# Kernel tuning notes

Hardware: AMD Instinct MI355X
Metric: run time of the kernel (lower is better)

Reference implementation:

```python
import jax, jax.numpy as jnp
import numpy as np

B, C, H, W = 2, 64, 256, 256
P = 3          # n_pyramids
NO = 16        # per-pyramid output channels
FEX = P * NO   # 48
N = 32768      # |yi| = mask.sum()


def _conv(x, w):
    return jax.lax.conv_general_dilated(
        x, w, window_strides=(1, 1), padding='SAME',
        dimension_numbers=('NCHW', 'OIHW', 'NCHW'))


def _mask_weight(mask):
    # MaskedConv: w = mask / clamp(avg3x3(mask), 1e-8)  (computed under no_grad)
    avg = jnp.ones((1, 1, 3, 3), mask.dtype) / 9.0
    wm = _conv(mask, avg)
    return jax.lax.stop_gradient(mask / jnp.clip(wm, 1e-8))


def _mconv(x, w, wm):
    return _conv(x, w) * wm


def _resblock(x, w1, w2, mask, wm):
    x = mask * x
    r = jax.nn.relu(_mconv(x, w1, wm))
    r = _mconv(r, w2, wm)
    return x + r


def setup_inputs() -> dict:
    key = jax.random.key(0)
    ks = jax.random.split(key, 12)
    rng = np.random.default_rng(0)
    yi_np = np.sort(rng.choice(H * W, size=N, replace=False)).astype(np.int32)
    mask_flat = np.zeros(H * W, np.float32)
    mask_flat[yi_np] = 1.0
    mask = jnp.asarray(mask_flat).reshape(1, 1, H, W)
    # near-identity homography (3x3)
    m = jnp.asarray(np.array([[0.9, 0.05, 2.0],
                              [-0.03, 1.1, -1.0],
                              [1e-4, -2e-4, 1.0]], np.float32))
    s = 0.05
    return {
        'xs': jax.random.normal(ks[0], (P, B, C, H, W), jnp.float32),
        'mask': mask,
        'yi': jnp.asarray(yi_np),
        'm': m,
        'ss_res_w': s * jax.random.normal(ks[1], (P, 2, 2, C, C, 3, 3), jnp.float32),
        'ss_out_w': s * jax.random.normal(ks[2], (P, NO, C, 3, 3), jnp.float32),
        'feat_res_w': s * jax.random.normal(ks[3], (2, 2, FEX, FEX, 3, 3), jnp.float32),
        'samp_w1': s * jax.random.normal(ks[4], (FEX, FEX + 1), jnp.float32),
        'samp_b1': s * jax.random.normal(ks[5], (FEX,), jnp.float32),
        'samp_w2': s * jax.random.normal(ks[6], (FEX, FEX), jnp.float32),
        'samp_b2': s * jax.random.normal(ks[7], (FEX,), jnp.float32),
        'samp_w3': s * jax.random.normal(ks[8], (P, FEX), jnp.float32),
        'samp_b3': s * jax.random.normal(ks[9], (P,), jnp.float32),
    }


def reference(xs, mask, yi, m, ss_res_w, ss_out_w, feat_res_w,
              samp_w1, samp_b1, samp_w2, samp_b2, samp_w3, samp_b3):
    wm = _mask_weight(mask)
    # ---- MSResFeature: per-pyramid MaskedResSeq(64->64->16, depth=3) ----
    feats = []
    for i in range(P):  # small fixed loop over pyramids
        x = mask * xs[i]
        x = _resblock(x, ss_res_w[i, 0, 0], ss_res_w[i, 0, 1], mask, wm)
        x = _resblock(x, ss_res_w[i, 1, 0], ss_res_w[i, 1, 1], mask, wm)
        x = _mconv(x, ss_out_w[i], wm)
        feats.append(x)
    f = jnp.concatenate(feats, axis=1)  # (B, 48, H, W)
    # shared trunk: MaskedResSeq(48->48->48, depth=3), residual
    g = mask * f
    g = _resblock(g, feat_res_w[0, 0], feat_res_w[0, 1], mask, wm)
    g = _resblock(g, feat_res_w[1, 0], feat_res_w[1, 1], mask, wm)
    f = f + g
    b = f.shape[0]
    # ---- gather at sparse indices yi ----
    ff = f.reshape(b, FEX, -1)[:, :, yi]  # (B, 48, N)
    # ---- dsda: |Jacobian det| of projective warp, log-scaled (no_grad) ----
    ygrid, xgrid = jnp.meshgrid(jnp.arange(H, dtype=f.dtype),
                                jnp.arange(W, dtype=f.dtype), indexing='ij')
    wcoord = m[2, 0] * xgrid + m[2, 1] * ygrid + m[2, 2]
    dsda = jnp.abs(jnp.linalg.det(m)) / jnp.clip(jnp.abs(wcoord), 1e-8) ** 3
    dsda = jnp.log(dsda.reshape(-1)[yi] + 1e-8)
    dsda = jax.lax.stop_gradient(jnp.broadcast_to(dsda[None, None, :], (b, 1, N)))
    h = jnp.concatenate((ff, dsda), axis=1)  # (B, 49, N)
    # ---- 1x1 Conv1d sampler MLP ----
    h = jax.nn.relu(jnp.einsum('oc,bcn->bon', samp_w1, h) + samp_b1[None, :, None])
    h = jax.nn.relu(jnp.einsum('oc,bcn->bon', samp_w2, h) + samp_b2[None, :, None])
    p = jnp.einsum('oc,bcn->bon', samp_w3, h) + samp_b3[None, :, None]  # (B, 3, N)
    # ---- scatter back to dense grid and blend pyramids ----
    ws = jnp.zeros((b, P, H * W), f.dtype).at[:, :, yi].set(p)
    ws = ws.reshape(b, P, H, W)
    out = jnp.sum(ws.transpose(1, 0, 2, 3)[:, :, None] * xs, axis=0)  # (B, C, H, W)
    return out
```

## Files before the change

kernel.cpp:

```cpp
#include <hip/hip_runtime.h>
#include <hip/hip_bf16.h>

typedef unsigned short ushort_t;
typedef __attribute__((ext_vector_type(8))) short short8;
typedef __attribute__((ext_vector_type(4))) short short4v;
typedef __attribute__((ext_vector_type(4))) float f32x4;

constexpr int Hh = 256, Ww = 256, HW = Hh * Ww;
constexpr int Bb = 2, Cc = 64, Pp = 3, NOo = 16, FEXc = 48, Nn = 32768;
constexpr int TW = 32, TH = 4;
constexpr int HALOP4 = 6 * 34;
constexpr int ASLOT = 26;
constexpr int PADH = 72;

__device__ inline ushort_t f2bf(float v) {
    __hip_bfloat16 h = __float2bfloat16(v);
    return *(ushort_t*)&h;
}
__device__ inline float bf2f(ushort_t u) {
    __hip_bfloat16 h = *(__hip_bfloat16*)&u;
    return __bfloat162float(h);
}
__device__ inline void gload_lds16(const ushort_t* g, ushort_t* l) {
    __builtin_amdgcn_global_load_lds(
        (const __attribute__((address_space(1))) unsigned int*)g,
        (__attribute__((address_space(3))) unsigned int*)l, 16, 0, 0);
}
template <int N>
__device__ __forceinline__ void wait_vm() {
    if constexpr (N == 0) asm volatile("s_waitcnt vmcnt(0)" ::: "memory");
    else if constexpr (N == 3) asm volatile("s_waitcnt vmcnt(3)" ::: "memory");
    else if constexpr (N == 5) asm volatile("s_waitcnt vmcnt(5)" ::: "memory");
}

__global__ __launch_bounds__(256) void k_wm(const float* __restrict__ mask,
                                            float* __restrict__ wm,
                                            float* __restrict__ zpage) {
    int pos = blockIdx.x * 256 + threadIdx.x;
    if (blockIdx.x == 0 && threadIdx.x < 64) zpage[threadIdx.x] = 0.f;
    int h = pos >> 8, w = pos & 255;
    float s = 0.f;
    #pragma unroll
    for (int dy = -1; dy <= 1; ++dy)
        #pragma unroll
        for (int dx = -1; dx <= 1; ++dx) {
            int hh = h + dy, ww = w + dx;
            if (hh >= 0 && hh < Hh && ww >= 0 && ww < Ww) s += mask[hh * Ww + ww];
        }
    float avg = s * (1.f / 9.f);
    wm[pos] = mask[pos] / fmaxf(avg, 1e-8f);
}

__global__ __launch_bounds__(256) void k_zero(float4* __restrict__ p) {
    p[blockIdx.x * 256 + threadIdx.x] = make_float4(0.f, 0.f, 0.f, 0.f);
}

__global__ __launch_bounds__(256) void k_wx_res(const float* __restrict__ src,
                                                ushort_t* __restrict__ dst) {
    int idx = blockIdx.x * 256 + threadIdx.x;
    int j = idx / 36864; int rem = idx - j * 36864;
    int t = rem >> 12; int o = (rem >> 6) & 63; int c = rem & 63;
    dst[idx] = f2bf(src[j * 36864 + o * 576 + c * 9 + t]);
}
__global__ __launch_bounds__(256) void k_wx_out(const float* __restrict__ src,
                                                ushort_t* __restrict__ dst) {
    int idx = blockIdx.x * 256 + threadIdx.x;
    int i = idx / 9216; int rem = idx - i * 9216;
    int t = rem >> 10; int o = (rem >> 6) & 15; int c = rem & 63;
    dst[idx] = f2bf(src[i * 9216 + o * 576 + c * 9 + t]);
}
__global__ __launch_bounds__(256) void k_wx_trunk(const float* __restrict__ src,
                                                  ushort_t* __restrict__ dst) {
    int idx = blockIdx.x * 256 + threadIdx.x;
    int j = idx / 27648; int rem = idx - j * 27648;
    int t = rem / 3072; int rem2 = rem - t * 3072;
    int o = rem2 >> 6; int c = rem2 & 63;
    float v = (c < 48) ? src[j * (48 * 48 * 9) + o * 432 + c * 9 + t] : 0.f;
    dst[idx] = f2bf(v);
}
__global__ __launch_bounds__(256) void k_wx_mlp(
    const float* __restrict__ w1, const float* __restrict__ b1,
    const float* __restrict__ w2, const float* __restrict__ b2,
    const float* __restrict__ w3, const float* __restrict__ b3,
    ushort_t* __restrict__ dst) {
    int idx = blockIdx.x * 256 + threadIdx.x;
    float v = 0.f;
    if (idx < 3072) {
        int o = idx >> 6, c = idx & 63;
        v = (c < 49) ? w1[o * 49 + c] : (c == 49 ? b1[o] : 0.f);
    } else if (idx < 6144) {
        int o = (idx - 3072) >> 6, c = idx & 63;
        v = (c < 48) ? w2[o * 48 + c] : (c == 48 ? b2[o] : 0.f);
    } else {
        int o = (idx - 6144) >> 6, c = idx & 63;
        if (o < 3) v = (c < 48) ? w3[o * 48 + c] : (c == 49 ? b3[o] : 0.f);
    }
    dst[idx] = f2bf(v);
}

__global__ __launch_bounds__(256) void k_xm(const float* __restrict__ xs,
                                            const float* __restrict__ mask,
                                            ushort_t* __restrict__ X) {
    __shared__ float l[64 * 65];
    const int p0 = blockIdx.x * 64;
    const size_t zoff = (size_t)blockIdx.y * 64 * HW;
    const int tid = threadIdx.x;
    const int px = tid & 63;
    const float mv = mask[p0 + px];
    #pragma unroll
    for (int k = 0; k < 16; ++k) {
        int c = (tid >> 6) + 4 * k;
        l[c * 65 + px] = xs[zoff + (size_t)c * HW + p0 + px] * mv;
    }
    __syncthreads();
    #pragma unroll
    for (int k = 0; k < 2; ++k) {
        int idx = tid + k * 256;
        int p = idx >> 3, c8 = idx & 7;
        short8 v;
        #pragma unroll
        for (int i = 0; i < 8; ++i) v[i] = (short)f2bf(l[(c8 * 8 + i) * 65 + p]);
        *(short8*)&X[zoff + (size_t)(p0 + p) * 64 + c8 * 8] = v;
    }
}

template <int OC, int MODE, bool TOF>
__global__ __launch_bounds__(256) void k_mconv(
    const ushort_t* __restrict__ in,
    const ushort_t* __restrict__ wgt, int wstride,
    const float* __restrict__ wm,
    const ushort_t* __restrict__ zp,
    const ushort_t* __restrict__ base,
    ushort_t* __restrict__ out) {
    constexpr int NG = (OC + 31) / 32;
    constexpr int NPH = 2 * NG;
    constexpr int WSLOT = (OC >= 48) ? 20 : 12;
    constexpr int WV = WSLOT / 4;
    extern __shared__ __align__(1024) ushort_t smem[];
    ushort_t* alds  = smem;
    ushort_t* wlds0 = smem + 208 * 64;
    ushort_t* wlds1 = wlds0 + WSLOT * 512;
    const int tid = threadIdx.x;
    const int wv = tid >> 6;
    const int ln = tid & 63;
    const int w0 = blockIdx.x * TW, h0 = blockIdx.y * TH;
    const int zz = blockIdx.z;
    const ushort_t* inb = in + (size_t)zz * HW * 64;
    const ushort_t* wB = wgt + (size_t)(zz >> 1) * wstride;
    const ushort_t* baseb = base ? base + (size_t)zz * HW * 64 : nullptr;
    ushort_t* outb = TOF ? out + (size_t)(zz & 1) * HW * 64 : out + (size_t)zz * HW * 64;
    const int ocb = TOF ? (zz >> 1) * 16 : 0;
    const int lo = ln & 15, slr = ln >> 4;

    auto wstage = [&](int p, ushort_t* wbuf) {
        const int gi = p >> 1, h = p & 1;
        const int ob = gi * 32;
        const int ocg = (OC - ob >= 32) ? 32 : 16;
        #pragma unroll
        for (int k = 0; k < WV; ++k) {
            int s = wv + 4 * k;
            int rl = s * 16 + (ln >> 2);
            int d = ln & 3;
            int j = d ^ ((rl ^ (rl >> 2)) & 3);
            int t, ol;
            if (ocg == 32) { t = rl >> 5; ol = rl & 31; }
            else           { t = rl >> 4; ol = rl & 15; }
            bool valid = rl < 9 * ocg;
            const ushort_t* src = valid
                ? wB + (size_t)(t * OC + ob + ol) * 64 + h * 32 + j * 8
                : wB + j * 8;
            gload_lds16(src, &wbuf[s * 512]);
        }
    };

    wstage(0, wlds0);
    #pragma unroll
    for (int k = 0; k < 7; ++k) {
        int s = wv + 4 * k;
        if (s < ASLOT) {
            int pp = s * 8 + (ln >> 3);
            int r = (pp * 241) >> 13;
            int col = pp - r * 34;
            int gh = h0 + r - 1, gw = w0 + col - 1;
            bool ok = (pp < HALOP4) & (gh >= 0) & (gh < Hh) & (gw >= 0) & (gw < Ww);
            int che = ((ln & 7) ^ (pp & 7)) << 3;
            const ushort_t* src = ok ? inb + (size_t)(gh * Ww + gw) * 64 + che : zp + che;
            gload_lds16(src, &alds[s * 512]);
        }
    }

    f32x4 acc[2][2];
    #pragma unroll
    for (int p = 0; p < NPH; ++p) {
        const int gi = p >> 1, h = p & 1;
        const int ob = gi * 32;
        const int ocg = (OC - ob >= 32) ? 32 : 16;
        const int nmg = ocg / 16;
        ushort_t* wcur = (p & 1) ? wlds1 : wlds0;
        if (p + 1 < NPH) {
            wstage(p + 1, (p & 1) ? wlds0 : wlds1);
            wait_vm<WV>();
        } else {
            wait_vm<0>();
        }
        __syncthreads();

        if (h == 0) {
            #pragma unroll
            for (int mfl = 0; mfl < 2; ++mfl)
                #pragma unroll
                for (int nf = 0; nf < 2; ++nf) acc[mfl][nf] = (f32x4){0.f, 0.f, 0.f, 0.f};
        }

        #pragma unroll
        for (int dy = 0; dy < 3; ++dy)
            #pragma unroll
            for (int dx = 0; dx < 3; ++dx) {
                const int t = dy * 3 + dx;
                short8 afr[2];
                #pragma unroll
                for (int mfl = 0; mfl < 2; ++mfl) if (mfl < nmg) {
                    int rl = t * ocg + mfl * 16 + lo;
                    afr[mfl] = *(const short8*)
                        &wcur[rl * 32 + ((slr ^ ((rl ^ (rl >> 2)) & 3)) << 3)];
                }
                short8 bfr[2];
                #pragma unroll
                for (int nf = 0; nf < 2; ++nf) {
                    int pp2 = (wv + dy) * 34 + nf * 16 + lo + dx;
                    bfr[nf] = *(const short8*)
                        &alds[pp2 * 64 + (((h * 4 + slr) ^ (pp2 & 7)) << 3)];
                }
                #pragma unroll
                for (int mfl = 0; mfl < 2; ++mfl) if (mfl < nmg)
                    #pragma unroll
                    for (int nf = 0; nf < 2; ++nf)
                        acc[mfl][nf] = __builtin_amdgcn_mfma_f32_16x16x32_bf16(
                            afr[mfl], bfr[nf], acc[mfl][nf], 0, 0, 0);
            }

        if (h == 1) {
            #pragma unroll
            for (int nf = 0; nf < 2; ++nf) {
                int r = h0 + wv;
                int x = w0 + nf * 16 + lo;
                int pos = r * Ww + x;
                float wmv = wm[pos];
                #pragma unroll
                for (int mfl = 0; mfl < 2; ++mfl) if (mfl < nmg) {
                    int o0 = ocb + ob + mfl * 16 + slr * 4;
                    size_t oi = (size_t)pos * 64 + o0;
                    float v[4];
                    #pragma unroll
                    for (int q = 0; q < 4; ++q) v[q] = acc[mfl][nf][q] * wmv;
                    if (MODE == 0) {
                        #pragma unroll
                        for (int q = 0; q < 4; ++q) v[q] = fmaxf(v[q], 0.f);
                    } else if (MODE == 1) {
                        short4v bv = *(const short4v*)&baseb[oi];
                        #pragma unroll
                        for (int q = 0; q < 4; ++q) v[q] += bf2f((ushort_t)bv[q]);
                    }
                    short4v sv;
                    #pragma unroll
                    for (int q = 0; q < 4; ++q) sv[q] = (short)f2bf(v[q]);
                    *(short4v*)&outb[oi] = sv;
                }
            }
        }
        if (p + 1 < NPH) __syncthreads();
    }
}

__global__ __launch_bounds__(256) void k_gather_mlp(
    const ushort_t* __restrict__ F, const ushort_t* __restrict__ G,
    const int* __restrict__ yi, const float* __restrict__ m,
    const ushort_t* __restrict__ wA1, const ushort_t* __restrict__ wA2,
    const ushort_t* __restrict__ wA3, float* __restrict__ pvd) {
    __shared__ __align__(16) ushort_t HA[4 * 16 * PADH];
    __shared__ __align__(16) ushort_t HB[4 * 16 * PADH];
    const int tid = threadIdx.x, wv = tid >> 6, ln = tid & 63;
    ushort_t* ha = HA + wv * 16 * PADH;
    ushort_t* hb = HB + wv * 16 * PADH;
    const int t0 = blockIdx.x * 64 + wv * 16;
    const int b = t0 >> 15;
    const int lo = ln & 15, g8 = (ln >> 4) * 8;

    #pragma unroll
    for (int rnd = 0; rnd < 2; ++rnd) {
        int j = rnd * 64 + ln;
        if (j < 96) {
            int pt = j / 6, sl = j - pt * 6;
            int n = (t0 + pt) & (Nn - 1);
            int pos = yi[n];
            size_t gi = ((size_t)(b * HW) + pos) * 64 + sl * 8;
            short8 fa = *(const short8*)&F[gi];
            short8 ga = *(const short8*)&G[gi];
            short8 sv;
            #pragma unroll
            for (int i = 0; i < 8; ++i)
                sv[i] = (short)f2bf(bf2f((ushort_t)fa[i]) + bf2f((ushort_t)ga[i]));
            *(short8*)&ha[pt * PADH + sl * 8] = sv;
        }
    }
    if (ln < 16) {
        int pt = ln;
        int n = (t0 + pt) & (Nn - 1);
        int pos = yi[n];
        float det = m[0] * (m[4] * m[8] - m[5] * m[7])
                  - m[1] * (m[3] * m[8] - m[5] * m[6])
                  + m[2] * (m[3] * m[7] - m[4] * m[6]);
        int yr = pos >> 8, xc = pos & 255;
        float wc = m[6] * (float)xc + m[7] * (float)yr + m[8];
        float cw = fmaxf(fabsf(wc), 1e-8f);
        float dsda = fabsf(det) / (cw * cw * cw);
        float ld = logf(dsda + 1e-8f);
        const ushort_t one = f2bf(1.0f);
        short8 z = {0, 0, 0, 0, 0, 0, 0, 0};
        short8 sa = z; sa[0] = (short)f2bf(ld); sa[1] = (short)one;
        short8 sb = z; sb[0] = (short)one;
        *(short8*)&ha[pt * PADH + 48] = sa;
        *(short8*)&ha[pt * PADH + 56] = z;
        *(short8*)&hb[pt * PADH + 48] = sb;
        *(short8*)&hb[pt * PADH + 56] = z;
    }
    asm volatile("s_waitcnt lgkmcnt(0)" ::: "memory");

    f32x4 a1[3] = {{0.f,0.f,0.f,0.f},{0.f,0.f,0.f,0.f},{0.f,0.f,0.f,0.f}};
    #pragma unroll
    for (int ks = 0; ks < 2; ++ks) {
        short8 bf = *(const short8*)&ha[lo * PADH + ks * 32 + g8];
        #pragma unroll
        for (int mf = 0; mf < 3; ++mf) {
            short8 af = *(const short8*)&wA1[(mf * 16 + lo) * 64 + ks * 32 + g8];
            a1[mf] = __builtin_amdgcn_mfma_f32_16x16x32_bf16(af, bf, a1[mf], 0, 0, 0);
        }
    }
    #pragma unroll
    for (int mf = 0; mf < 3; ++mf) {
        short4v sv;
        #pragma unroll
        for (int j = 0; j < 4; ++j) sv[j] = (short)f2bf(fmaxf(a1[mf][j], 0.f));
        *(short4v*)&hb[lo * PADH + mf * 16 + (ln >> 4) * 4] = sv;
    }
    asm volatile("s_waitcnt lgkmcnt(0)" ::: "memory");

    f32x4 a2[3] = {{0.f,0.f,0.f,0.f},{0.f,0.f,0.f,0.f},{0.f,0.f,0.f,0.f}};
    #pragma unroll
    for (int ks = 0; ks < 2; ++ks) {
        short8 bf = *(const short8*)&hb[lo * PADH + ks * 32 + g8];
        #pragma unroll
        for (int mf = 0; mf < 3; ++mf) {
            short8 af = *(const short8*)&wA2[(mf * 16 + lo) * 64 + ks * 32 + g8];
            a2[mf] = __builtin_amdgcn_mfma_f32_16x16x32_bf16(af, bf, a2[mf], 0, 0, 0);
        }
    }
    #pragma unroll
    for (int mf = 0; mf < 3; ++mf) {
        short4v sv;
        #pragma unroll
        for (int j = 0; j < 4; ++j) sv[j] = (short)f2bf(fmaxf(a2[mf][j], 0.f));
        *(short4v*)&ha[lo * PADH + mf * 16 + (ln >> 4) * 4] = sv;
    }
    asm volatile("s_waitcnt lgkmcnt(0)" ::: "memory");

    f32x4 a3 = {0.f, 0.f, 0.f, 0.f};
    #pragma unroll
    for (int ks = 0; ks < 2; ++ks) {
        short8 bf = *(const short8*)&ha[lo * PADH + ks * 32 + g8];
        short8 af = *(const short8*)&wA3[lo * 64 + ks * 32 + g8];
        a3 = __builtin_amdgcn_mfma_f32_16x16x32_bf16(af, bf, a3, 0, 0, 0);
    }
    if (ln < 16) {
        int n = (t0 + lo) & (Nn - 1);
        int pos = yi[n];
        #pragma unroll
        for (int j = 0; j < 3; ++j)
            pvd[(size_t)(b * Pp + j) * HW + pos] = a3[j];
    }
}

__global__ __launch_bounds__(256) void k_blend(const float4* __restrict__ xs,
                                               const float4* __restrict__ pvd,
                                               float4* __restrict__ out) {
    int i = blockIdx.x * 256 + threadIdx.x;
    int pos4 = i & (HW / 4 - 1);
    int bc = i >> 14;
    int b = bc >> 6;
    float4 acc = make_float4(0.f, 0.f, 0.f, 0.f);
    #pragma unroll
    for (int p = 0; p < Pp; ++p) {
        float4 pv = pvd[(b * Pp + p) * (HW / 4) + pos4];
        float4 x = xs[p * (Bb * Cc * HW / 4) + i];
        acc.x += pv.x * x.x;
        acc.y += pv.y * x.y;
        acc.z += pv.z * x.z;
        acc.w += pv.w * x.w;
    }
    out[i] = acc;
}

extern "C" void kernel_launch(void* const* d_in, const int* in_sizes, int n_in,
                              void* d_out, int out_size, void* d_ws, size_t ws_size,
                              hipStream_t stream) {
    const float* xs        = (const float*)d_in[0];
    const float* mask      = (const float*)d_in[1];
    const int*   yi        = (const int*)d_in[2];
    const float* m         = (const float*)d_in[3];
    const float* ss_res_w  = (const float*)d_in[4];
    const float* ss_out_w  = (const float*)d_in[5];
    const float* feat_res_w= (const float*)d_in[6];
    const float* w1 = (const float*)d_in[7];
    const float* b1 = (const float*)d_in[8];
    const float* w2 = (const float*)d_in[9];
    const float* b2 = (const float*)d_in[10];
    const float* w3 = (const float*)d_in[11];
    const float* b3 = (const float*)d_in[12];

    float* wm    = (float*)d_ws;
    float* zpage = wm + HW;
    float* pvd   = zpage + 64;
    ushort_t* wB = (ushort_t*)(pvd + (size_t)Bb * Pp * HW);
    constexpr size_t RES_T = 12 * 9 * 64 * 64;
    constexpr size_t OUT_T = 3 * 9 * 16 * 64;
    constexpr size_t TRK_T = 4 * 9 * 48 * 64;
    constexpr size_t MLP_T = 7168;
    constexpr size_t ZT = (size_t)Pp * Bb * HW * 64;
    ushort_t* wA = wB + RES_T + OUT_T + TRK_T;
    ushort_t* X = wA + MLP_T;
    ushort_t* U = X + ZT;
    ushort_t* V = U + ZT;
    ushort_t* F = V + ZT;
    ushort_t* G = F + (size_t)Bb * HW * 64;
    const ushort_t* zp = (const ushort_t*)zpage;

    k_wm<<<HW / 256, 256, 0, stream>>>(mask, wm, zpage);
    k_wx_res  <<<RES_T / 256, 256, 0, stream>>>(ss_res_w, wB);
    k_wx_out  <<<OUT_T / 256, 256, 0, stream>>>(ss_out_w, wB + RES_T);
    k_wx_trunk<<<TRK_T / 256, 256, 0, stream>>>(feat_res_w, wB + RES_T + OUT_T);
    k_wx_mlp  <<<MLP_T / 256, 256, 0, stream>>>(w1, b1, w2, b2, w3, b3, wA);

    const dim3 gridP(Ww / TW, Hh / TH, Pp * Bb);
    const dim3 gridT(Ww / TW, Hh / TH, Bb);
    const int RS = 4 * 9 * 64 * 64;
    const int OS = 9 * 16 * 64;
    constexpr size_t SH64 = 26624 + 2 * 20 * 1024;
    constexpr size_t SH48 = SH64;
    constexpr size_t SH16 = 26624 + 2 * 12 * 1024;

    k_xm<<<dim3(HW / 64, Pp * Bb), 256, 0, stream>>>(xs, mask, X);
    k_mconv<64, 0, false><<<gridP, 256, SH64, stream>>>(X, wB,             RS, wm, zp, nullptr, U);
    k_mconv<64, 1, false><<<gridP, 256, SH64, stream>>>(U, wB + 1 * 36864, RS, wm, zp, X,       V);
    k_mconv<64, 0, false><<<gridP, 256, SH64, stream>>>(V, wB + 2 * 36864, RS, wm, zp, nullptr, U);
    k_mconv<64, 1, false><<<gridP, 256, SH64, stream>>>(U, wB + 3 * 36864, RS, wm, zp, V,       V);
    k_mconv<16, 2, true ><<<gridP, 256, SH16, stream>>>(V, wB + RES_T,     OS, wm, zp, nullptr, F);

    const ushort_t* tw = wB + RES_T + OUT_T;
    k_mconv<48, 0, false><<<gridT, 256, SH48, stream>>>(F, tw,             0, wm, zp, nullptr, U);
    k_mconv<48, 1, false><<<gridT, 256, SH48, stream>>>(U, tw + 1 * 27648, 0, wm, zp, F,       G);
    k_mconv<48, 0, false><<<gridT, 256, SH48, stream>>>(G, tw + 2 * 27648, 0, wm, zp, nullptr, U);
    k_mconv<48, 1, false><<<gridT, 256, SH48, stream>>>(U, tw + 3 * 27648, 0, wm, zp, G,       G);

    k_zero<<<(Bb * Pp * HW / 4) / 256, 256, 0, stream>>>((float4*)pvd);
    k_gather_mlp<<<Bb * Nn / 64, 256, 0, stream>>>(F, G, yi, m,
        wA, wA + 3072, wA + 6144, pvd);
    k_blend<<<(Bb * Cc * HW / 4) / 256, 256, 0, stream>>>((const float4*)xs, (const float4*)pvd,
                                                          (float4*)d_out);
}
```

Measured before the change: 340.1 us.

## Fuse each residual block's two masked convs into one halo-recompute kernel

Adds a k_pair kernel that computes both 3x3 masked convolutions of a residual block in one launch. It loads a 2-pixel halo tile, computes the first conv plus ReLU over the expanded region into LDS, then runs the second conv from LDS and adds the residual read from the staged input. This removes the intermediate global write and read and halves the conv launches. In exchange it recomputes halo work, serializes weight staging (the double-buffered waits become vmcnt(0)), and uses more LDS and accumulator registers per block, which can lower occupancy.

```diff
diff --git a/kernel.cpp b/kernel.cpp
--- a/kernel.cpp
+++ b/kernel.cpp
@@ -11,6 +11,7 @@
 constexpr int TW = 32, TH = 4;
 constexpr int HALOP4 = 6 * 34;
 constexpr int ASLOT = 26;
+constexpr int ITROWS = 288;
 constexpr int PADH = 72;
 
 __device__ inline ushort_t f2bf(float v) {
@@ -26,11 +27,8 @@
         (const __attribute__((address_space(1))) unsigned int*)g,
         (__attribute__((address_space(3))) unsigned int*)l, 16, 0, 0);
 }
-template <int N>
-__device__ __forceinline__ void wait_vm() {
-    if constexpr (N == 0) asm volatile("s_waitcnt vmcnt(0)" ::: "memory");
-    else if constexpr (N == 3) asm volatile("s_waitcnt vmcnt(3)" ::: "memory");
-    else if constexpr (N == 5) asm volatile("s_waitcnt vmcnt(5)" ::: "memory");
+__device__ __forceinline__ void wait_vm0() {
+    asm volatile("s_waitcnt vmcnt(0)" ::: "memory");
 }
 
 __global__ __launch_bounds__(256) void k_wm(const float* __restrict__ mask,
@@ -121,6 +119,198 @@
         #pragma unroll
         for (int i = 0; i < 8; ++i) v[i] = (short)f2bf(l[(c8 * 8 + i) * 65 + p]);
         *(short8*)&X[zoff + (size_t)(p0 + p) * 64 + c8 * 8] = v;
+    }
+}
+
+template <int OC>
+__global__ __launch_bounds__(256) void k_pair(
+    const ushort_t* __restrict__ in,
+    const ushort_t* __restrict__ wgt, int wstride,
+    const float* __restrict__ wm,
+    const ushort_t* __restrict__ zp,
+    ushort_t* __restrict__ out) {
+    constexpr int NM = OC / 16;
+    constexpr int WROWS = 9 * OC;
+    constexpr int WDMA = WROWS / 16;
+    constexpr int C2OFF = 9 * OC * 64;
+    extern __shared__ __align__(1024) ushort_t smem[];
+    ushort_t* alds = smem;
+    ushort_t* mlds = smem;
+    ushort_t* wlds = smem + ITROWS * 64;
+    const int tid = threadIdx.x, wv = tid >> 6, ln = tid & 63;
+    const int lo = ln & 15, slr = ln >> 4;
+    const int w0 = blockIdx.x * TW, h0 = blockIdx.y * TH;
+    const int zz = blockIdx.z;
+    const ushort_t* inb = in + (size_t)zz * HW * 64;
+    ushort_t* outb = out + (size_t)zz * HW * 64;
+    const ushort_t* wg1 = wgt + (size_t)(zz >> 1) * wstride;
+    const ushort_t* wg2 = wg1 + C2OFF;
+
+    auto wstage = [&](const ushort_t* ws, int h) {
+        #pragma unroll
+        for (int k = 0; k < (WDMA + 3) / 4; ++k) {
+            int s = wv + 4 * k;
+            if (s < WDMA) {
+                int rl = s * 16 + (ln >> 2);
+                int d = ln & 3;
+                int j = d ^ ((rl ^ (rl >> 2)) & 3);
+                gload_lds16(ws + (size_t)rl * 64 + h * 32 + j * 8, &wlds[s * 512]);
+            }
+        }
+    };
+
+    wstage(wg1, 0);
+    #pragma unroll
+    for (int k = 0; k < 9; ++k) {
+        int s = wv * 9 + k;
+        int pp = s * 8 + (ln >> 3);
+        int r = (pp * 228) >> 13;
+        int col = pp - r * 36;
+        int gh = h0 + r - 2, gw = w0 + col - 2;
+        bool ok = (gh >= 0) & (gh < Hh) & (gw >= 0) & (gw < Ww);
+        int che = ((ln & 7) ^ (pp & 7)) << 3;
+        const ushort_t* src = ok ? inb + (size_t)(gh * Ww + gw) * 64 + che : zp + che;
+        gload_lds16(src, &alds[s * 512]);
+    }
+    wait_vm0();
+    __syncthreads();
+
+    f32x4 a1[6][3];
+    #pragma unroll
+    for (int mr = 0; mr < 6; ++mr)
+        #pragma unroll
+        for (int cf = 0; cf < 3; ++cf) a1[mr][cf] = (f32x4){0.f, 0.f, 0.f, 0.f};
+
+    #pragma unroll
+    for (int h = 0; h < 2; ++h) {
+        if (h) {
+            __syncthreads();
+            wstage(wg1, 1);
+            wait_vm0();
+            __syncthreads();
+        }
+        if (wv < NM) {
+            #pragma unroll
+            for (int dy = 0; dy < 3; ++dy)
+                #pragma unroll
+                for (int dx = 0; dx < 3; ++dx) {
+                    const int t = dy * 3 + dx;
+                    int rl = t * OC + wv * 16 + lo;
+                    short8 af = *(const short8*)
+                        &wlds[rl * 32 + ((slr ^ ((rl ^ (rl >> 2)) & 3)) << 3)];
+                    #pragma unroll
+                    for (int mr = 0; mr < 6; ++mr)
+                        #pragma unroll
+                        for (int cf = 0; cf < 3; ++cf) {
+                            int cc = cf * 16 + lo + dx;
+                            if (cf == 2) cc = min(cc, 35);
+                            int pp2 = (mr + dy) * 36 + cc;
+                            short8 b = *(const short8*)
+                                &alds[pp2 * 64 + (((h * 4 + slr) ^ (pp2 & 7)) << 3)];
+                            a1[mr][cf] = __builtin_amdgcn_mfma_f32_16x16x32_bf16(
+                                af, b, a1[mr][cf], 0, 0, 0);
+                        }
+                }
+        }
+    }
+
+    short4v bres[2][4];
+    #pragma unroll
+    for (int nf = 0; nf < 2; ++nf) {
+        int ppb = (wv + 2) * 36 + nf * 16 + lo + 2;
+        #pragma unroll
+        for (int mf = 0; mf < 4; ++mf) if (mf < NM) {
+            int o0 = mf * 16 + slr * 4;
+            bres[nf][mf] = *(const short4v*)
+                &alds[ppb * 64 + (((o0 >> 3) ^ (ppb & 7)) << 3) + (slr & 1) * 4];
+        }
+    }
+    __syncthreads();
+
+    if (wv < NM) {
+        #pragma unroll
+        for (int mr = 0; mr < 6; ++mr)
+            #pragma unroll
+            for (int cf = 0; cf < 3; ++cf) {
+                int mc = cf * 16 + lo;
+                if (mc < 34) {
+                    int gh = h0 + mr - 1, gw = w0 + mc - 1;
+                    bool ok = (gh >= 0) & (gh < Hh) & (gw >= 0) & (gw < Ww);
+                    float wmv = ok ? wm[gh * Ww + gw] : 0.f;
+                    int mpx = mr * 34 + mc;
+                    int o0 = wv * 16 + slr * 4;
+                    short4v sv;
+                    #pragma unroll
+                    for (int q = 0; q < 4; ++q)
+                        sv[q] = (short)f2bf(fmaxf(a1[mr][cf][q] * wmv, 0.f));
+                    *(short4v*)&mlds[mpx * 64 + (((o0 >> 3) ^ (mpx & 7)) << 3) + (slr & 1) * 4] = sv;
+                }
+            }
+    }
+    __syncthreads();
+    wstage(wg2, 0);
+    wait_vm0();
+    __syncthreads();
+
+    f32x4 a2[4][2];
+    #pragma unroll
+    for (int mf = 0; mf < 4; ++mf)
+        #pragma unroll
+        for (int nf = 0; nf < 2; ++nf) a2[mf][nf] = (f32x4){0.f, 0.f, 0.f, 0.f};
+
+    #pragma unroll
+    for (int h = 0; h < 2; ++h) {
+        if (h) {
+            __syncthreads();
+            wstage(wg2, 1);
+            wait_vm0();
+            __syncthreads();
+        }
+        #pragma unroll
+        for (int dy = 0; dy < 3; ++dy)
+            #pragma unroll
+            for (int dx = 0; dx < 3; ++dx) {
+                const int t = dy * 3 + dx;
+                short8 afr[4];
+                #pragma unroll
+                for (int mf = 0; mf < 4; ++mf) if (mf < NM) {
+                    int rl = t * OC + mf * 16 + lo;
+                    afr[mf] = *(const short8*)
+                        &wlds[rl * 32 + ((slr ^ ((rl ^ (rl >> 2)) & 3)) << 3)];
+                }
+                short8 bfr[2];
+                #pragma unroll
+                for (int nf = 0; nf < 2; ++nf) {
+                    int pp2 = (wv + dy) * 34 + nf * 16 + lo + dx;
+                    bfr[nf] = *(const short8*)
+                        &mlds[pp2 * 64 + (((h * 4 + slr) ^ (pp2 & 7)) << 3)];
+                }
+                #pragma unroll
+                for (int mf = 0; mf < 4; ++mf) if (mf < NM)
+                    #pragma unroll
+                    for (int nf = 0; nf < 2; ++nf)
+                        a2[mf][nf] = __builtin_amdgcn_mfma_f32_16x16x32_bf16(
+                            afr[mf], bfr[nf], a2[mf][nf], 0, 0, 0);
+            }
+    }
+
+    #pragma unroll
+    for (int nf = 0; nf < 2; ++nf) {
+        int pos = (h0 + wv) * Ww + w0 + nf * 16 + lo;
+        float wmv = wm[pos];
+        #pragma unroll
+        for (int mf = 0; mf < 4; ++mf) if (mf < NM) {
+            int o0 = mf * 16 + slr * 4;
+            size_t oi = (size_t)pos * 64 + o0;
+            float v[4];
+            #pragma unroll
+            for (int q = 0; q < 4; ++q)
+                v[q] = a2[mf][nf][q] * wmv + bf2f((ushort_t)bres[nf][mf][q]);
+            short4v sv;
+            #pragma unroll
+            for (int q = 0; q < 4; ++q) sv[q] = (short)f2bf(v[q]);
+            *(short4v*)&outb[oi] = sv;
+        }
     }
 }
 
@@ -197,12 +387,8 @@
         const int ocg = (OC - ob >= 32) ? 32 : 16;
         const int nmg = ocg / 16;
         ushort_t* wcur = (p & 1) ? wlds1 : wlds0;
-        if (p + 1 < NPH) {
-            wstage(p + 1, (p & 1) ? wlds0 : wlds1);
-            wait_vm<WV>();
-        } else {
-            wait_vm<0>();
-        }
+        if (p + 1 < NPH) wstage(p + 1, (p & 1) ? wlds0 : wlds1);
+        wait_vm0();
         __syncthreads();
 
         if (h == 0) {
@@ -242,9 +428,7 @@
         if (h == 1) {
             #pragma unroll
             for (int nf = 0; nf < 2; ++nf) {
-                int r = h0 + wv;
-                int x = w0 + nf * 16 + lo;
-                int pos = r * Ww + x;
+                int pos = (h0 + wv) * Ww + w0 + nf * 16 + lo;
                 float wmv = wm[pos];
                 #pragma unroll
                 for (int mfl = 0; mfl < 2; ++mfl) if (mfl < nmg) {
@@ -444,22 +628,17 @@
     const dim3 gridT(Ww / TW, Hh / TH, Bb);
     const int RS = 4 * 9 * 64 * 64;
     const int OS = 9 * 16 * 64;
-    constexpr size_t SH64 = 26624 + 2 * 20 * 1024;
-    constexpr size_t SH48 = SH64;
-    constexpr size_t SH16 = 26624 + 2 * 12 * 1024;
+    constexpr size_t PSH64 = (size_t)ITROWS * 128 + 9 * 64 * 64;
+    constexpr size_t PSH48 = (size_t)ITROWS * 128 + 9 * 48 * 64;
+    constexpr size_t SH16  = 26624 + 2 * 12 * 1024;
 
     k_xm<<<dim3(HW / 64, Pp * Bb), 256, 0, stream>>>(xs, mask, X);
-    k_mconv<64, 0, false><<<gridP, 256, SH64, stream>>>(X, wB,             RS, wm, zp, nullptr, U);
-    k_mconv<64, 1, false><<<gridP, 256, SH64, stream>>>(U, wB + 1 * 36864, RS, wm, zp, X,       V);
-    k_mconv<64, 0, false><<<gridP, 256, SH64, stream>>>(V, wB + 2 * 36864, RS, wm, zp, nullptr, U);
-    k_mconv<64, 1, false><<<gridP, 256, SH64, stream>>>(U, wB + 3 * 36864, RS, wm, zp, V,       V);
-    k_mconv<16, 2, true ><<<gridP, 256, SH16, stream>>>(V, wB + RES_T,     OS, wm, zp, nullptr, F);
-
+    k_pair<64><<<gridP, 256, PSH64, stream>>>(X, wB,             RS, wm, zp, V);
+    k_pair<64><<<gridP, 256, PSH64, stream>>>(V, wB + 2 * 36864, RS, wm, zp, U);
+    k_mconv<16, 2, true><<<gridP, 256, SH16, stream>>>(U, wB + RES_T, OS, wm, zp, nullptr, F);
     const ushort_t* tw = wB + RES_T + OUT_T;
-    k_mconv<48, 0, false><<<gridT, 256, SH48, stream>>>(F, tw,             0, wm, zp, nullptr, U);
-    k_mconv<48, 1, false><<<gridT, 256, SH48, stream>>>(U, tw + 1 * 27648, 0, wm, zp, F,       G);
-    k_mconv<48, 0, false><<<gridT, 256, SH48, stream>>>(G, tw + 2 * 27648, 0, wm, zp, nullptr, U);
-    k_mconv<48, 1, false><<<gridT, 256, SH48, stream>>>(U, tw + 3 * 27648, 0, wm, zp, G,       G);
+    k_pair<48><<<gridT, 256, PSH48, stream>>>(F, tw,             0, wm, zp, U);
+    k_pair<48><<<gridT, 256, PSH48, stream>>>(U, tw + 2 * 27648, 0, wm, zp, G);
 
     k_zero<<<(Bb * Pp * HW / 4) / 256, 256, 0, stream>>>((float4*)pvd);
     k_gather_mlp<<<Bb * Nn / 64, 256, 0, stream>>>(F, G, yi, m,
```

Result: slower. 523.5 us (+53.9%).
